# Performance work log

Hardware: AMD Instinct MI355X
Metric: run time of the kernel (lower is better)

Reference implementation:

```python
import jax, jax.numpy as jnp
import numpy as np

B, C, H, W = 4, 64, 256, 256
HEADS, WS, DIL = 4, 3, 2
HD = C // HEADS            # 16
HID = 256
EPS = 1e-5
PAD = DIL * (WS // 2)      # 2
K = WS * WS                # 9 neighbors


def setup_inputs() -> dict:
    key = jax.random.key(0)
    ks = jax.random.split(key, 8)
    s = 0.05
    return {
        "x": jax.random.normal(ks[0], (B, C, H, W), jnp.float32),
        "gamma1": jnp.ones((C,), jnp.float32),
        "beta1": jnp.zeros((C,), jnp.float32),
        "gamma2": jnp.ones((C,), jnp.float32),
        "beta2": jnp.zeros((C,), jnp.float32),
        "w_qkv": jax.random.normal(ks[1], (3 * C, C), jnp.float32) * s,
        "b_qkv": jax.random.normal(ks[2], (3 * C,), jnp.float32) * s,
        "w_out": jax.random.normal(ks[3], (C, C), jnp.float32) * s,
        "b_out": jax.random.normal(ks[4], (C,), jnp.float32) * s,
        "w1": jax.random.normal(ks[5], (HID, C), jnp.float32) * s,
        "b1": jax.random.normal(ks[6], (HID,), jnp.float32) * s,
        "w2": jax.random.normal(ks[7], (C, HID), jnp.float32) * s,
        "b2": jnp.zeros((C,), jnp.float32),
    }


def _ln(x, g, b):
    # LayerNorm over channel dim of [B,C,H,W]
    mu = jnp.mean(x, axis=1, keepdims=True)
    var = jnp.mean(jnp.square(x - mu), axis=1, keepdims=True)
    xn = (x - mu) * jax.lax.rsqrt(var + EPS)
    return xn * g[None, :, None, None] + b[None, :, None, None]


def _conv1x1(x, w, b):
    # x: [B,Cin,H,W], w: [Cout,Cin]
    y = jnp.einsum('bchw,oc->bohw', x, w)
    return y + b[None, :, None, None]


def _gather_neighbors(t):
    # t: [B,heads,H,W,hd] -> [B,heads,H,W,K,hd] with zero boundary padding
    tp = jnp.pad(t, ((0, 0), (0, 0), (PAD, PAD), (PAD, PAD), (0, 0)))
    views = [tp[:, :, i * DIL:i * DIL + H, j * DIL:j * DIL + W, :]
             for i in range(WS) for j in range(WS)]
    return jnp.stack(views, axis=4)


def _attn(x, w_qkv, b_qkv, w_out, b_out):
    qkv = _conv1x1(x, w_qkv, b_qkv)                       # [B,3C,H,W]
    qkv = qkv.reshape(B, 3, HEADS, HD, H, W)
    qkv = jnp.transpose(qkv, (1, 0, 2, 4, 5, 3))          # [3,B,heads,H,W,hd]
    q, k, v = qkv[0], qkv[1], qkv[2]
    k_nb = _gather_neighbors(k)                           # [B,heads,H,W,K,hd]
    v_nb = _gather_neighbors(v)
    scale = HD ** -0.5
    scores = jnp.einsum('bnhwd,bnhwkd->bnhwk', q * scale, k_nb)
    attn = jax.nn.softmax(scores, axis=-1)
    out = jnp.einsum('bnhwk,bnhwkd->bnhwd', attn, v_nb)   # [B,heads,H,W,hd]
    out = jnp.transpose(out, (0, 1, 4, 2, 3)).reshape(B, C, H, W)
    return _conv1x1(out, w_out, b_out)


def reference(x, gamma1, beta1, gamma2, beta2, w_qkv, b_qkv, w_out, b_out, w1, b1, w2, b2):
    # pre-norm: x = x + attn(norm1(x)); x = x + mlp(norm2(x))
    x = x + _attn(_ln(x, gamma1, beta1), w_qkv, b_qkv, w_out, b_out)
    h = jax.nn.gelu(_conv1x1(_ln(x, gamma2, beta2), w1, b1), approximate=False)
    m = jax.nn.gelu(_conv1x1(h, w2, b2), approximate=False)
    return x + m
```

## Files before the change

### kernel.cpp

```cpp
#include <hip/hip_runtime.h>
#include <math.h>

#define HW    65536
#define EPSLN 1e-5f

typedef unsigned short ushort_t;
typedef __attribute__((ext_vector_type(8))) short bf16x8;
typedef __attribute__((ext_vector_type(4))) short bf16x4;
typedef __attribute__((ext_vector_type(4))) float f32x4;

#define QKV_USHORTS (4*192*65536)
#define WQ_H 0
#define WQ_L 12288
#define W1_H 24576
#define W1_L 40960
#define W2_H 57344
#define W2_L 73728
#define WO_H 90112
#define WO_L 94208

__device__ __forceinline__ ushort_t f2bf(float f) {
    unsigned u = __float_as_uint(f);
    return (ushort_t)((u + 0x7FFFu + ((u >> 16) & 1u)) >> 16);
}
__device__ __forceinline__ float bf2f(ushort_t h) {
    return __uint_as_float(((unsigned)h) << 16);
}
__device__ __forceinline__ float gelu_fast(float v) {
    float u  = v * v * v;
    float z2 = 1.5957691216057308f * v + 0.07135481627283788f * u;
    float e  = __expf(z2);
    float th = 1.f - 2.f * __builtin_amdgcn_rcpf(1.f + e);
    return 0.5f * v * (1.f + th);
}

__global__ void k_prep(const float* __restrict__ wq, const float* __restrict__ w1,
                       const float* __restrict__ w2, const float* __restrict__ wo,
                       ushort_t* __restrict__ wb)
{
    int i = blockIdx.x * 256 + threadIdx.x;
    float v; int oh, ol;
    if (i < 12288)      { v = wq[i];          oh = WQ_H + i;          ol = WQ_L + i; }
    else if (i < 28672) { int j = i - 12288;  v = w1[j]; oh = W1_H+j; ol = W1_L+j; }
    else if (i < 45056) { int j = i - 28672;  v = w2[j]; oh = W2_H+j; ol = W2_L+j; }
    else                { int j = i - 45056;  v = wo[j]; oh = WO_H+j; ol = WO_L+j; }
    ushort_t h = f2bf(v);
    wb[oh] = h;
    wb[ol] = f2bf(v - bf2f(h));
}

__global__ __launch_bounds__(64, 5) void k_lnqkv_mfma(
    const float* __restrict__ x,  const float* __restrict__ g1,
    const float* __restrict__ b1, const ushort_t* __restrict__ wb,
    const float* __restrict__ bq, ushort_t* __restrict__ qkv)
{
    __shared__ float sg1[64], sb1[64], sbq[192];
    int tid = threadIdx.x;
    sg1[tid] = g1[tid]; sb1[tid] = b1[tid];
#pragma unroll
    for (int i = tid; i < 192; i += 64) sbq[i] = bq[i];
    __syncthreads();

    int lane = tid;
    int g = lane >> 4, q = lane & 15;
    int px0 = blockIdx.x * 64;
    int b   = px0 >> 16;
    int hwb = px0 & 65535;
    const float* xb = x + (size_t)b * 64 * HW;

    bf16x8 bh[4][2];
#pragma unroll
    for (int pg = 0; pg < 4; ++pg) {
        int hw = hwb + pg * 16 + q;
        const float* xp = xb + hw;
        float xv[16];
#pragma unroll
        for (int j = 0; j < 8; ++j) {
            xv[j]     = xp[(g * 8 + j) * HW];
            xv[8 + j] = xp[(32 + g * 8 + j) * HW];
        }
        float s = 0.f;
#pragma unroll
        for (int j = 0; j < 16; ++j) s += xv[j];
        s += __shfl_xor(s, 16); s += __shfl_xor(s, 32);
        float mu = s * 0.015625f;
        float s2 = 0.f;
#pragma unroll
        for (int j = 0; j < 16; ++j) { float d = xv[j] - mu; s2 += d * d; }
        s2 += __shfl_xor(s2, 16); s2 += __shfl_xor(s2, 32);
        float inv = rsqrtf(s2 * 0.015625f + EPSLN);
#pragma unroll
        for (int kt = 0; kt < 2; ++kt)
#pragma unroll
            for (int j = 0; j < 8; ++j) {
                int c = kt * 32 + g * 8 + j;
                float f = (xv[kt * 8 + j] - mu) * inv * sg1[c] + sb1[c];
                bh[pg][kt][j] = (short)f2bf(f);
            }
    }

    const ushort_t* wqh = wb + WQ_H;
    const ushort_t* wql = wb + WQ_L;
    ushort_t* outb = qkv + (size_t)b * 12 * HW * 16;

#pragma unroll 2
    for (int mt = 0; mt < 12; ++mt) {
        bf16x8 ah[2], al[2];
#pragma unroll
        for (int kt = 0; kt < 2; ++kt) {
            ah[kt] = *(const bf16x8*)(wqh + (mt * 16 + q) * 64 + kt * 32 + g * 8);
            al[kt] = *(const bf16x8*)(wql + (mt * 16 + q) * 64 + kt * 32 + g * 8);
        }
        f32x4 bias = *(const f32x4*)(&sbq[mt * 16 + 4 * g]);
#pragma unroll
        for (int pg = 0; pg < 4; ++pg) {
            f32x4 d = bias;
#pragma unroll
            for (int kt = 0; kt < 2; ++kt) {
                d = __builtin_amdgcn_mfma_f32_16x16x32_bf16(ah[kt], bh[pg][kt], d, 0, 0, 0);
                d = __builtin_amdgcn_mfma_f32_16x16x32_bf16(al[kt], bh[pg][kt], d, 0, 0, 0);
            }
            bf16x4 st;
#pragma unroll
            for (int i = 0; i < 4; ++i) st[i] = (short)f2bf(d[i]);
            int hw = hwb + pg * 16 + q;
            *(bf16x4*)(outb + ((size_t)mt * HW + hw) * 16 + 4 * g) = st;
        }
    }
}

__global__ __launch_bounds__(64, 4) void k_attn_mfma(
    const float* __restrict__ x, const ushort_t* __restrict__ qkv,
    const ushort_t* __restrict__ wb, const float* __restrict__ bo,
    float* __restrict__ x1)
{
    __shared__ ushort_t abuf[64 * 64];
    __shared__ float sbo[64];
    int lane = threadIdx.x;
    sbo[lane] = bo[lane];
    __syncthreads();

    int px = blockIdx.x * 64 + lane;
    int b = px >> 16, hw = px & 65535;
    int hh = hw >> 8, ww = hw & 255;
    const ushort_t* tb = qkv + (size_t)b * 12 * HW * 16;

    int   nidx[9];
    float nmask[9];
#pragma unroll
    for (int n = 0; n < 9; ++n) {
        int dy = (n / 3) * 2 - 2, dx = (n % 3) * 2 - 2;
        int y = hh + dy, xw = ww + dx;
        int yc = min(max(y, 0), 255), xc = min(max(xw, 0), 255);
        nidx[n]  = yc * 256 + xc;
        nmask[n] = (y == yc && xw == xc) ? 1.f : 0.f;
    }

#pragma unroll 1
    for (int head = 0; head < 4; ++head) {
        const ushort_t* qp = tb + ((size_t)head * HW + hw) * 16;
        bf16x8 q0 = *(const bf16x8*)qp;
        bf16x8 q1 = *(const bf16x8*)(qp + 8);
        float qv[16];
#pragma unroll
        for (int j = 0; j < 8; ++j) {
            qv[j]     = bf2f((ushort_t)q0[j]) * 0.25f;
            qv[8 + j] = bf2f((ushort_t)q1[j]) * 0.25f;
        }
        const ushort_t* kb = tb + (size_t)(4 + head) * HW * 16;
        const ushort_t* vb = tb + (size_t)(8 + head) * HW * 16;

        float sc[9];
#pragma unroll
        for (int n = 0; n < 9; ++n) {
            const ushort_t* kp = kb + (size_t)nidx[n] * 16;
            bf16x8 k0 = *(const bf16x8*)kp;
            bf16x8 k1 = *(const bf16x8*)(kp + 8);
            float s = 0.f;
#pragma unroll
            for (int j = 0; j < 8; ++j) {
                s += qv[j]     * bf2f((ushort_t)k0[j]);
                s += qv[8 + j] * bf2f((ushort_t)k1[j]);
            }
            sc[n] = s * nmask[n];
        }
        float mx = sc[0];
#pragma unroll
        for (int n = 1; n < 9; ++n) mx = fmaxf(mx, sc[n]);

        float ew[9], sum = 0.f;
#pragma unroll
        for (int n = 0; n < 9; ++n) {
            float e = __expf(sc[n] - mx);
            sum += e;
            ew[n] = e * nmask[n];
        }

        float o16[16];
#pragma unroll
        for (int d = 0; d < 16; ++d) o16[d] = 0.f;
#pragma unroll
        for (int n = 0; n < 9; ++n) {
            const ushort_t* vp = vb + (size_t)nidx[n] * 16;
            bf16x8 v0 = *(const bf16x8*)vp;
            bf16x8 v1 = *(const bf16x8*)(vp + 8);
            float a = ew[n];
#pragma unroll
            for (int j = 0; j < 8; ++j) {
                o16[j]     += a * bf2f((ushort_t)v0[j]);
                o16[8 + j] += a * bf2f((ushort_t)v1[j]);
            }
        }
        float isum = __builtin_amdgcn_rcpf(sum);

        bf16x8 w0, w1v;
#pragma unroll
        for (int j = 0; j < 8; ++j) {
            w0[j]  = (short)f2bf(o16[j] * isum);
            w1v[j] = (short)f2bf(o16[8 + j] * isum);
        }
        int c0 = (head * 2)     ^ (lane & 7);
        int c1 = (head * 2 + 1) ^ (lane & 7);
        *(bf16x8*)(&abuf[lane * 64 + c0 * 8]) = w0;
        *(bf16x8*)(&abuf[lane * 64 + c1 * 8]) = w1v;
    }
    __syncthreads();

    int g = lane >> 4, q = lane & 15;
    const ushort_t* woh = wb + WO_H;
    const ushort_t* wol = wb + WO_L;
    int hwwb = (blockIdx.x * 64) & 65535;
    const float* xb = x + (size_t)b * 64 * HW;
    float* x1b = x1 + (size_t)b * 64 * HW;

    bf16x8 bb[4][2];
#pragma unroll
    for (int pg = 0; pg < 4; ++pg) {
        int r = pg * 16 + q;
#pragma unroll
        for (int kt = 0; kt < 2; ++kt) {
            int c = (kt * 4 + g) ^ (r & 7);
            bb[pg][kt] = *(const bf16x8*)(&abuf[r * 64 + c * 8]);
        }
    }

#pragma unroll 1
    for (int mt = 0; mt < 4; ++mt) {
        bf16x8 ah[2], al[2];
#pragma unroll
        for (int kt = 0; kt < 2; ++kt) {
            ah[kt] = *(const bf16x8*)(woh + (mt * 16 + q) * 64 + kt * 32 + g * 8);
            al[kt] = *(const bf16x8*)(wol + (mt * 16 + q) * 64 + kt * 32 + g * 8);
        }
        f32x4 bias = *(const f32x4*)(&sbo[mt * 16 + 4 * g]);
#pragma unroll
        for (int pg = 0; pg < 4; ++pg) {
            f32x4 d = bias;
#pragma unroll
            for (int kt = 0; kt < 2; ++kt) {
                d = __builtin_amdgcn_mfma_f32_16x16x32_bf16(ah[kt], bb[pg][kt], d, 0, 0, 0);
                d = __builtin_amdgcn_mfma_f32_16x16x32_bf16(al[kt], bb[pg][kt], d, 0, 0, 0);
            }
            int hwg = hwwb + pg * 16 + q;
#pragma unroll
            for (int i = 0; i < 4; ++i) {
                int o = mt * 16 + 4 * g + i;
                x1b[(size_t)o * HW + hwg] = xb[(size_t)o * HW + hwg] + d[i];
            }
        }
    }
}

__global__ __launch_bounds__(64, 6) void k_mlp_mfma(
    const float* __restrict__ g2, const float* __restrict__ b2,
    const ushort_t* __restrict__ wb,
    const float* __restrict__ bb1, const float* __restrict__ bb2,
    float* __restrict__ io)
{
    __shared__ ushort_t hbh[2][2048];
    __shared__ float sg2[64], sb2[64], sbb1[256], sbb2[64];
    int tid = threadIdx.x;
    sg2[tid] = g2[tid]; sb2[tid] = b2[tid]; sbb2[tid] = bb2[tid];
#pragma unroll
    for (int i = tid; i < 256; i += 64) sbb1[i] = bb1[i];
    __syncthreads();

    int lane = tid;
    int g = lane >> 4, q = lane & 15;
    int px0 = blockIdx.x * 64;
    int b   = px0 >> 16;
    int hwb = px0 & 65535;
    float* iob = io + (size_t)b * 64 * HW;

    bf16x8 bh[4][2];
#pragma unroll
    for (int pg = 0; pg < 4; ++pg) {
        int hw = hwb + pg * 16 + q;
        const float* xp = iob + hw;
        float xv[16];
#pragma unroll
        for (int j = 0; j < 8; ++j) {
            xv[j]     = xp[(g * 8 + j) * HW];
            xv[8 + j] = xp[(32 + g * 8 + j) * HW];
        }
        float s = 0.f;
#pragma unroll
        for (int j = 0; j < 16; ++j) s += xv[j];
        s += __shfl_xor(s, 16); s += __shfl_xor(s, 32);
        float mu = s * 0.015625f;
        float s2 = 0.f;
#pragma unroll
        for (int j = 0; j < 16; ++j) { float d = xv[j] - mu; s2 += d * d; }
        s2 += __shfl_xor(s2, 16); s2 += __shfl_xor(s2, 32);
        float inv = rsqrtf(s2 * 0.015625f + EPSLN);
#pragma unroll
        for (int kt = 0; kt < 2; ++kt)
#pragma unroll
            for (int j = 0; j < 8; ++j) {
                int c = kt * 32 + g * 8 + j;
                float f = (xv[kt * 8 + j] - mu) * inv * sg2[c] + sb2[c];
                bh[pg][kt][j] = (short)f2bf(f);
            }
    }

    const ushort_t* w1h = wb + W1_H;  const ushort_t* w1l = wb + W1_L;
    const ushort_t* w2h = wb + W2_H;  const ushort_t* w2l = wb + W2_L;

    f32x4 acc2[4][4];
#pragma unroll
    for (int m2 = 0; m2 < 4; ++m2) {
        f32x4 binit = *(const f32x4*)(&sbb2[m2 * 16 + 4 * g]);
#pragma unroll
        for (int pg = 0; pg < 4; ++pg) acc2[pg][m2] = binit;
    }

#pragma unroll 1
    for (int mtp = 0; mtp < 8; ++mtp) {
        int buf = mtp & 1;
#pragma unroll
        for (int e = 0; e < 2; ++e) {
            int mt = mtp * 2 + e;
            bf16x8 ah[2], al[2];
#pragma unroll
            for (int kt = 0; kt < 2; ++kt) {
                ah[kt] = *(const bf16x8*)(w1h + (mt * 16 + q) * 64 + kt * 32 + g * 8);
                al[kt] = *(const bf16x8*)(w1l + (mt * 16 + q) * 64 + kt * 32 + g * 8);
            }
            f32x4 b1v = *(const f32x4*)(&sbb1[mt * 16 + 4 * g]);
            int chunk = (e * 4 + g) ^ (q & 6);
#pragma unroll
            for (int pg = 0; pg < 4; ++pg) {
                f32x4 d = b1v;
#pragma unroll
                for (int kt = 0; kt < 2; ++kt) {
                    d = __builtin_amdgcn_mfma_f32_16x16x32_bf16(ah[kt], bh[pg][kt], d, 0, 0, 0);
                    d = __builtin_amdgcn_mfma_f32_16x16x32_bf16(al[kt], bh[pg][kt], d, 0, 0, 0);
                }
                bf16x4 vh;
#pragma unroll
                for (int i = 0; i < 4; ++i)
                    vh[i] = (short)f2bf(gelu_fast(d[i]));
                *(bf16x4*)(&hbh[buf][pg * 512 + q * 32 + chunk * 4]) = vh;
            }
        }
        int c0 = (2 * g) ^ (q & 6);
        bf16x8 p2[4];
#pragma unroll
        for (int pg = 0; pg < 4; ++pg)
            p2[pg] = *(const bf16x8*)(&hbh[buf][pg * 512 + q * 32 + c0 * 4]);
#pragma unroll
        for (int m2 = 0; m2 < 4; ++m2) {
            bf16x8 ah2 = *(const bf16x8*)(w2h + (m2 * 16 + q) * 256 + mtp * 32 + g * 8);
            bf16x8 al2 = *(const bf16x8*)(w2l + (m2 * 16 + q) * 256 + mtp * 32 + g * 8);
#pragma unroll
            for (int pg = 0; pg < 4; ++pg) {
                acc2[pg][m2] = __builtin_amdgcn_mfma_f32_16x16x32_bf16(ah2, p2[pg], acc2[pg][m2], 0, 0, 0);
                acc2[pg][m2] = __builtin_amdgcn_mfma_f32_16x16x32_bf16(al2, p2[pg], acc2[pg][m2], 0, 0, 0);
            }
        }
    }

#pragma unroll
    for (int pg = 0; pg < 4; ++pg)
#pragma unroll
        for (int m2 = 0; m2 < 4; ++m2)
#pragma unroll
            for (int i = 0; i < 4; ++i) {
                int o = m2 * 16 + 4 * g + i;
                int hw = hwb + pg * 16 + q;
                float m = gelu_fast(acc2[pg][m2][i]);
                iob[(size_t)o * HW + hw] = iob[(size_t)o * HW + hw] + m;
            }
}

extern "C" void kernel_launch(void* const* d_in, const int* in_sizes, int n_in,
                              void* d_out, int out_size, void* d_ws, size_t ws_size,
                              hipStream_t stream)
{
    const float* x     = (const float*)d_in[0];
    const float* g1    = (const float*)d_in[1];
    const float* b1    = (const float*)d_in[2];
    const float* g2    = (const float*)d_in[3];
    const float* b2    = (const float*)d_in[4];
    const float* w_qkv = (const float*)d_in[5];
    const float* b_qkv = (const float*)d_in[6];
    const float* w_out = (const float*)d_in[7];
    const float* b_out = (const float*)d_in[8];
    const float* w1    = (const float*)d_in[9];
    const float* bb1   = (const float*)d_in[10];
    const float* w2    = (const float*)d_in[11];
    const float* bb2   = (const float*)d_in[12];

    float*    out = (float*)d_out;
    ushort_t* qkv = (ushort_t*)d_ws;
    ushort_t* wb  = (ushort_t*)d_ws + QKV_USHORTS;

    k_prep      <<<192,  256, 0, stream>>>(w_qkv, w1, w2, w_out, wb);
    k_lnqkv_mfma<<<4096, 64, 0, stream>>>(x, g1, b1, wb, b_qkv, qkv);
    k_attn_mfma <<<4096, 64, 0, stream>>>(x, qkv, wb, b_out, out);
    k_mlp_mfma  <<<4096, 64, 0, stream>>>(g2, b2, wb, bb1, bb2, out);
}
```

Before: 292.3 us.

## Fuse attention output projection with LN2 and MLP into one kernel

Merges the attention kernel and the MLP kernel into a single kernel per 64-pixel tile. The post-attention residual x1 stays in registers and feeds LayerNorm2 and the MLP through LDS, so x1 is never written to and reread from global memory. One kernel launch and about 2×64MB of fp32 traffic go away. In exchange the fused kernel holds more registers (x1r plus the MLP accumulators), which lowers the launch bound to 2 waves per SIMD and may reduce occupancy and latency hiding.

```diff
diff --git a/kernel.cpp b/kernel.cpp
--- a/kernel.cpp
+++ b/kernel.cpp
@@ -129,15 +129,20 @@
     }
 }
 
-__global__ __launch_bounds__(64, 4) void k_attn_mfma(
+__global__ __launch_bounds__(64, 2) void k_attn_mlp(
     const float* __restrict__ x, const ushort_t* __restrict__ qkv,
     const ushort_t* __restrict__ wb, const float* __restrict__ bo,
-    float* __restrict__ x1)
+    const float* __restrict__ g2, const float* __restrict__ b2,
+    const float* __restrict__ bb1, const float* __restrict__ bb2,
+    float* __restrict__ out)
 {
-    __shared__ ushort_t abuf[64 * 64];
-    __shared__ float sbo[64];
+    __shared__ ushort_t lds[4096];
+    __shared__ float sbo[64], sg2[64], sb2[64], sbb1[256], sbb2[64];
     int lane = threadIdx.x;
-    sbo[lane] = bo[lane];
+    sbo[lane] = bo[lane]; sg2[lane] = g2[lane];
+    sb2[lane] = b2[lane]; sbb2[lane] = bb2[lane];
+#pragma unroll
+    for (int i = lane; i < 256; i += 64) sbb1[i] = bb1[i];
     __syncthreads();
 
     int px = blockIdx.x * 64 + lane;
@@ -221,29 +226,29 @@
         }
         int c0 = (head * 2)     ^ (lane & 7);
         int c1 = (head * 2 + 1) ^ (lane & 7);
-        *(bf16x8*)(&abuf[lane * 64 + c0 * 8]) = w0;
-        *(bf16x8*)(&abuf[lane * 64 + c1 * 8]) = w1v;
+        *(bf16x8*)(&lds[lane * 64 + c0 * 8]) = w0;
+        *(bf16x8*)(&lds[lane * 64 + c1 * 8]) = w1v;
     }
     __syncthreads();
 
     int g = lane >> 4, q = lane & 15;
+    int hwb = (blockIdx.x * 64) & 65535;
+    const float* xb = x + (size_t)b * 64 * HW;
+
+    bf16x8 bbf[4][2];
+#pragma unroll
+    for (int pg = 0; pg < 4; ++pg) {
+        int r = pg * 16 + q;
+#pragma unroll
+        for (int kt = 0; kt < 2; ++kt) {
+            int c = (kt * 4 + g) ^ (r & 7);
+            bbf[pg][kt] = *(const bf16x8*)(&lds[r * 64 + c * 8]);
+        }
+    }
+
     const ushort_t* woh = wb + WO_H;
     const ushort_t* wol = wb + WO_L;
-    int hwwb = (blockIdx.x * 64) & 65535;
-    const float* xb = x + (size_t)b * 64 * HW;
-    float* x1b = x1 + (size_t)b * 64 * HW;
-
-    bf16x8 bb[4][2];
-#pragma unroll
-    for (int pg = 0; pg < 4; ++pg) {
-        int r = pg * 16 + q;
-#pragma unroll
-        for (int kt = 0; kt < 2; ++kt) {
-            int c = (kt * 4 + g) ^ (r & 7);
-            bb[pg][kt] = *(const bf16x8*)(&abuf[r * 64 + c * 8]);
-        }
-    }
-
+    f32x4 x1r[4][4];
 #pragma unroll 1
     for (int mt = 0; mt < 4; ++mt) {
         bf16x8 ah[2], al[2];
@@ -258,70 +263,63 @@
             f32x4 d = bias;
 #pragma unroll
             for (int kt = 0; kt < 2; ++kt) {
-                d = __builtin_amdgcn_mfma_f32_16x16x32_bf16(ah[kt], bb[pg][kt], d, 0, 0, 0);
-                d = __builtin_amdgcn_mfma_f32_16x16x32_bf16(al[kt], bb[pg][kt], d, 0, 0, 0);
-            }
-            int hwg = hwwb + pg * 16 + q;
+                d = __builtin_amdgcn_mfma_f32_16x16x32_bf16(ah[kt], bbf[pg][kt], d, 0, 0, 0);
+                d = __builtin_amdgcn_mfma_f32_16x16x32_bf16(al[kt], bbf[pg][kt], d, 0, 0, 0);
+            }
+            int hwg = hwb + pg * 16 + q;
 #pragma unroll
             for (int i = 0; i < 4; ++i) {
                 int o = mt * 16 + 4 * g + i;
-                x1b[(size_t)o * HW + hwg] = xb[(size_t)o * HW + hwg] + d[i];
-            }
-        }
-    }
-}
-
-__global__ __launch_bounds__(64, 6) void k_mlp_mfma(
-    const float* __restrict__ g2, const float* __restrict__ b2,
-    const ushort_t* __restrict__ wb,
-    const float* __restrict__ bb1, const float* __restrict__ bb2,
-    float* __restrict__ io)
-{
-    __shared__ ushort_t hbh[2][2048];
-    __shared__ float sg2[64], sb2[64], sbb1[256], sbb2[64];
-    int tid = threadIdx.x;
-    sg2[tid] = g2[tid]; sb2[tid] = b2[tid]; sbb2[tid] = bb2[tid];
-#pragma unroll
-    for (int i = tid; i < 256; i += 64) sbb1[i] = bb1[i];
-    __syncthreads();
-
-    int lane = tid;
-    int g = lane >> 4, q = lane & 15;
-    int px0 = blockIdx.x * 64;
-    int b   = px0 >> 16;
-    int hwb = px0 & 65535;
-    float* iob = io + (size_t)b * 64 * HW;
-
-    bf16x8 bh[4][2];
+                x1r[pg][mt][i] = xb[(size_t)o * HW + hwg] + d[i];
+            }
+        }
+    }
+    __syncthreads();
+
 #pragma unroll
     for (int pg = 0; pg < 4; ++pg) {
-        int hw = hwb + pg * 16 + q;
-        const float* xp = iob + hw;
-        float xv[16];
-#pragma unroll
-        for (int j = 0; j < 8; ++j) {
-            xv[j]     = xp[(g * 8 + j) * HW];
-            xv[8 + j] = xp[(32 + g * 8 + j) * HW];
-        }
         float s = 0.f;
 #pragma unroll
-        for (int j = 0; j < 16; ++j) s += xv[j];
+        for (int mt = 0; mt < 4; ++mt)
+#pragma unroll
+            for (int i = 0; i < 4; ++i) s += x1r[pg][mt][i];
         s += __shfl_xor(s, 16); s += __shfl_xor(s, 32);
         float mu = s * 0.015625f;
         float s2 = 0.f;
 #pragma unroll
-        for (int j = 0; j < 16; ++j) { float d = xv[j] - mu; s2 += d * d; }
+        for (int mt = 0; mt < 4; ++mt)
+#pragma unroll
+            for (int i = 0; i < 4; ++i) { float d = x1r[pg][mt][i] - mu; s2 += d * d; }
         s2 += __shfl_xor(s2, 16); s2 += __shfl_xor(s2, 32);
         float inv = rsqrtf(s2 * 0.015625f + EPSLN);
-#pragma unroll
-        for (int kt = 0; kt < 2; ++kt)
-#pragma unroll
-            for (int j = 0; j < 8; ++j) {
-                int c = kt * 32 + g * 8 + j;
-                float f = (xv[kt * 8 + j] - mu) * inv * sg2[c] + sb2[c];
-                bh[pg][kt][j] = (short)f2bf(f);
-            }
-    }
+
+        int r = pg * 16 + q;
+#pragma unroll
+        for (int mt = 0; mt < 4; ++mt) {
+            bf16x4 st;
+#pragma unroll
+            for (int i = 0; i < 4; ++i) {
+                int c = mt * 16 + 4 * g + i;
+                float f = (x1r[pg][mt][i] - mu) * inv * sg2[c] + sb2[c];
+                st[i] = (short)f2bf(f);
+            }
+            int chunk = (mt * 4 + g) ^ (q & 6);
+            *(bf16x4*)(&lds[r * 64 + chunk * 4]) = st;
+        }
+    }
+    __syncthreads();
+
+    bf16x8 bh[4][2];
+#pragma unroll
+    for (int pg = 0; pg < 4; ++pg) {
+        int r = pg * 16 + q;
+#pragma unroll
+        for (int kt = 0; kt < 2; ++kt) {
+            int c0 = (kt * 8 + 2 * g) ^ (q & 6);
+            bh[pg][kt] = *(const bf16x8*)(&lds[r * 64 + c0 * 4]);
+        }
+    }
+    __syncthreads();
 
     const ushort_t* w1h = wb + W1_H;  const ushort_t* w1l = wb + W1_L;
     const ushort_t* w2h = wb + W2_H;  const ushort_t* w2l = wb + W2_L;
@@ -360,14 +358,14 @@
 #pragma unroll
                 for (int i = 0; i < 4; ++i)
                     vh[i] = (short)f2bf(gelu_fast(d[i]));
-                *(bf16x4*)(&hbh[buf][pg * 512 + q * 32 + chunk * 4]) = vh;
+                *(bf16x4*)(&lds[buf * 2048 + pg * 512 + q * 32 + chunk * 4]) = vh;
             }
         }
         int c0 = (2 * g) ^ (q & 6);
         bf16x8 p2[4];
 #pragma unroll
         for (int pg = 0; pg < 4; ++pg)
-            p2[pg] = *(const bf16x8*)(&hbh[buf][pg * 512 + q * 32 + c0 * 4]);
+            p2[pg] = *(const bf16x8*)(&lds[buf * 2048 + pg * 512 + q * 32 + c0 * 4]);
 #pragma unroll
         for (int m2 = 0; m2 < 4; ++m2) {
             bf16x8 ah2 = *(const bf16x8*)(w2h + (m2 * 16 + q) * 256 + mtp * 32 + g * 8);
@@ -380,17 +378,19 @@
         }
     }
 
-#pragma unroll
-    for (int pg = 0; pg < 4; ++pg)
+    float* ob = out + (size_t)b * 64 * HW;
+#pragma unroll
+    for (int pg = 0; pg < 4; ++pg) {
+        int hwg = hwb + pg * 16 + q;
 #pragma unroll
         for (int m2 = 0; m2 < 4; ++m2)
 #pragma unroll
             for (int i = 0; i < 4; ++i) {
                 int o = m2 * 16 + 4 * g + i;
-                int hw = hwb + pg * 16 + q;
                 float m = gelu_fast(acc2[pg][m2][i]);
-                iob[(size_t)o * HW + hw] = iob[(size_t)o * HW + hw] + m;
-            }
+                ob[(size_t)o * HW + hwg] = x1r[pg][m2][i] + m;
+            }
+    }
 }
 
 extern "C" void kernel_launch(void* const* d_in, const int* in_sizes, int n_in,
@@ -417,6 +417,5 @@
 
     k_prep      <<<192,  256, 0, stream>>>(w_qkv, w1, w2, w_out, wb);
     k_lnqkv_mfma<<<4096, 64, 0, stream>>>(x, g1, b1, wb, b_qkv, qkv);
-    k_attn_mfma <<<4096, 64, 0, stream>>>(x, qkv, wb, b_out, out);
-    k_mlp_mfma  <<<4096, 64, 0, stream>>>(g2, b2, wb, bb1, bb2, out);
-}
+    k_attn_mlp  <<<4096, 64, 0, stream>>>(x, qkv, wb, b_out, g2, b2, bb1, bb2, out);
+}
```

New measurement: 329.3 us. +12.7%, slower.
